# Performance work log

Measured on AMD Instinct MI355X. Metric: run time of the kernel, lower is better.

Reference implementation:

```python
import math
import jax, jax.numpy as jnp
import numpy as np

MAX_ATOMS_PER_BB = 8

def _sinusoidal_pe(d_model, max_len):
    # Faithful port of SinusoidalPositionalEmbedding buffer construction.
    position = jnp.arange(max_len, dtype=jnp.float32)[:, None]          # (L,1)
    div_term = jnp.exp(jnp.arange(0, d_model, 2, dtype=jnp.float32) * -(math.log(10000.0) / d_model))
    n_even = math.ceil(d_model / 2)
    n_odd = d_model - n_even
    pe = jnp.zeros((max_len, d_model), dtype=jnp.float32)
    pe = pe.at[:, 0::2].set(jnp.sin(position * div_term[:n_even]))
    pe = pe.at[:, 1::2].set(jnp.cos(position * div_term[:n_odd]))
    return pe

def setup_inputs() -> dict:
    key = jax.random.key(0)
    k1, k2, k3, k4 = jax.random.split(key, 4)
    bs, n, dy, dc = 8, 32, 64, 256
    E = jax.random.normal(k1, (bs, n, n, dy), dtype=jnp.float32)
    e_mask1 = (jax.random.uniform(k2, (bs, n, 1, 1)) > 0.2).astype(jnp.float32)
    e_mask2 = (jax.random.uniform(k3, (bs, 1, n, 1)) > 0.2).astype(jnp.float32)
    W = jax.random.normal(k4, (dc, dy), dtype=jnp.float32) * (1.0 / math.sqrt(dy))
    return {"E": E, "e_mask1": e_mask1, "e_mask2": e_mask2, "W": W}

def reference(E, e_mask1, e_mask2, W):
    M = MAX_ATOMS_PER_BB
    bs, n, _, dy = E.shape
    nm = n * M
    # Positional embedding table indexed by arange(M*M).reshape(M,M) -> (M,M,dy)
    pe = _sinusoidal_pe(dy, M * M).reshape(M, M, dy)
    # Masks: note original flattening orders (n,M) for mask1 but (M,n) for mask2.
    mask1 = jnp.broadcast_to(e_mask1, (bs, n, M, 1)).reshape(bs, nm, 1, 1)
    mask2 = jnp.broadcast_to(e_mask2, (bs, M, n, 1)).reshape(bs, 1, nm, 1)
    mask = mask1 * mask2                                             # (bs,nm,nm,1)
    # Broadcast E (bs,n,1,n,1,dy) + pe (1,1,M,1,M,dy) -> (bs,n,M,n,M,dy)
    Eb = E[:, :, None, :, None, :] + pe[None, None, :, None, :, :]
    E_masked = Eb.reshape(bs, nm, nm, dy) * mask
    out = jnp.einsum('bijd,cd->bijc', E_masked, W)                    # (bs,nm,nm,dc)
    return out
```

## Files before the change

### kernel.cpp

```cpp
#include <hip/hip_runtime.h>
#include <math.h>

typedef float f32x4 __attribute__((ext_vector_type(4)));


__global__ __launch_bounds__(256) void prep_kernel(const float* __restrict__ W,
                                                   float* __restrict__ Cpe,
                                                   float* __restrict__ Wt) {
    const int pos = blockIdx.x;
    const int t   = threadIdx.x;
    Wt[pos * 256 + t] = W[t * 64 + pos];
    __shared__ float peL[64];
    if (t < 64) {
        const float k2  = (float)(t & ~1);
        const float div = expf(-k2 * (logf(10000.0f) / 64.0f));
        const float arg = (float)pos * div;
        peL[t] = (t & 1) ? cosf(arg) : sinf(arg);
    }
    __syncthreads();
    const f32x4* W4 = (const f32x4*)W;
    float acc = 0.0f;
#pragma unroll
    for (int d4 = 0; d4 < 16; ++d4) {
        f32x4 w = W4[t * 16 + d4];
        acc += w.x * peL[4 * d4 + 0] + w.y * peL[4 * d4 + 1] +
               w.z * peL[4 * d4 + 2] + w.w * peL[4 * d4 + 3];
    }
    Cpe[pos * 256 + t] = acc;
}

__global__ __launch_bounds__(256) void etoc_stream(const float* __restrict__ E,
                                                   const float* __restrict__ m1p,
                                                   const float* __restrict__ m2p,
                                                   const float* __restrict__ Wt,
                                                   const float* __restrict__ Cpe,
                                                   float* __restrict__ out) {
    const int blk = blockIdx.x;
    const int h = blk & 1;
    const int i = (blk >> 1) & 31;
    const int b = blk >> 6;
    const int t = threadIdx.x;
    const int w = t >> 6;
    const int g = t & 63;
    const int j0 = h * 16 + w * 4;

    const f32x4* Wt4 = (const f32x4*)Wt;
    const f32x4* E4  = (const f32x4*)E;
    const int ebase = ((b * 32 + i) * 32 + j0) * 16;
    f32x4 acc0 = {0,0,0,0}, acc1 = {0,0,0,0}, acc2 = {0,0,0,0}, acc3 = {0,0,0,0};
#pragma unroll 4
    for (int d4 = 0; d4 < 16; ++d4) {
        const f32x4 e0 = E4[ebase + 0 * 16 + d4];
        const f32x4 e1 = E4[ebase + 1 * 16 + d4];
        const f32x4 e2 = E4[ebase + 2 * 16 + d4];
        const f32x4 e3 = E4[ebase + 3 * 16 + d4];
#pragma unroll
        for (int dd = 0; dd < 4; ++dd) {
            const f32x4 wv = Wt4[(d4 * 4 + dd) * 64 + g];
            acc0 += wv * e0[dd];
            acc1 += wv * e1[dd];
            acc2 += wv * e2[dd];
            acc3 += wv * e3[dd];
        }
    }

    const float m1v = m1p[b * 32 + i];
    f32x4 mm[8];
    const f32x4* m2v = (const f32x4*)(m2p + b * 32);
#pragma unroll
    for (int k = 0; k < 8; ++k) mm[k] = m2v[k] * m1v;

    const f32x4* Cpe4 = (const f32x4*)Cpe;
    f32x4* out4 = (f32x4*)out;
    const size_t rowb = ((size_t)(b * 256 + i * 8) * 256 + (size_t)j0 * 8);

#pragma unroll 1
    for (int a = 0; a < 8; ++a) {
        f32x4 q[8];
#pragma unroll
        for (int c = 0; c < 8; ++c) q[c] = Cpe4[(a * 8 + c) * 64 + g];
#pragma unroll
        for (int jl = 0; jl < 4; ++jl) {
            const f32x4 ce = (jl == 0) ? acc0 : (jl == 1) ? acc1 : (jl == 2) ? acc2 : acc3;
            const size_t base = (rowb + (size_t)a * 256 + (size_t)jl * 8) * 64 + (size_t)g;
#pragma unroll
            for (int c = 0; c < 8; ++c) {
                const float m = mm[2 * jl + (c >> 2)][c & 3];
                f32x4 r = (ce + q[c]) * m;
                out4[base + (size_t)c * 64] = r;
            }
        }
    }
}

extern "C" void kernel_launch(void* const* d_in, const int* in_sizes, int n_in,
                              void* d_out, int out_size, void* d_ws, size_t ws_size,
                              hipStream_t stream) {
    const float* E   = (const float*)d_in[0];
    const float* m1p = (const float*)d_in[1];
    const float* m2p = (const float*)d_in[2];
    const float* W   = (const float*)d_in[3];
    float* out = (float*)d_out;

    float* Cpe = (float*)d_ws;
    float* Wt  = (float*)((char*)d_ws + 65536);

    prep_kernel<<<64, 256, 0, stream>>>(W, Cpe, Wt);
    etoc_stream<<<512, 256, 0, stream>>>(E, m1p, m2p, Wt, Cpe, out);
}
```

Baseline: 110.3 us.

## Split output rows across blocks with per-block pe row and nontemporal stores

Each block now owns one (b, i, a) output row instead of a (b, i, half) slice that looped over all 8 a-values. Each wave handles 8 j columns, so the E×W projection is recomputed 8× more often across blocks. In exchange there are 4× more blocks, contiguous 64 KB row writes and one Cpe load per block. Block IDs are swizzled so that blocks with the same (b, i) are spread out. Output writes use nontemporal stores to avoid polluting the cache. The trade-off is more redundant FMA work and E reads against better parallelism and store streaming.

```diff
diff --git a/kernel.cpp b/kernel.cpp
--- a/kernel.cpp
+++ b/kernel.cpp
@@ -35,32 +35,31 @@
                                                    const float* __restrict__ Wt,
                                                    const float* __restrict__ Cpe,
                                                    float* __restrict__ out) {
-    const int blk = blockIdx.x;
-    const int h = blk & 1;
-    const int i = (blk >> 1) & 31;
-    const int b = blk >> 6;
+    const int bid = blockIdx.x;
+    const int blk = (bid & 7) * 256 + (bid >> 3);
+    const int ii = blk & 255;
+    const int b  = blk >> 8;
+    const int i = ii >> 3, a = ii & 7;
     const int t = threadIdx.x;
     const int w = t >> 6;
     const int g = t & 63;
-    const int j0 = h * 16 + w * 4;
 
     const f32x4* Wt4 = (const f32x4*)Wt;
     const f32x4* E4  = (const f32x4*)E;
-    const int ebase = ((b * 32 + i) * 32 + j0) * 16;
-    f32x4 acc0 = {0,0,0,0}, acc1 = {0,0,0,0}, acc2 = {0,0,0,0}, acc3 = {0,0,0,0};
+    const int ebase = ((b * 32 + i) * 32 + w * 8) * 16;
+    f32x4 acc[8];
+#pragma unroll
+    for (int jl = 0; jl < 8; ++jl) acc[jl] = (f32x4){0, 0, 0, 0};
 #pragma unroll 4
     for (int d4 = 0; d4 < 16; ++d4) {
-        const f32x4 e0 = E4[ebase + 0 * 16 + d4];
-        const f32x4 e1 = E4[ebase + 1 * 16 + d4];
-        const f32x4 e2 = E4[ebase + 2 * 16 + d4];
-        const f32x4 e3 = E4[ebase + 3 * 16 + d4];
+        f32x4 e[8];
+#pragma unroll
+        for (int jl = 0; jl < 8; ++jl) e[jl] = E4[ebase + jl * 16 + d4];
 #pragma unroll
         for (int dd = 0; dd < 4; ++dd) {
             const f32x4 wv = Wt4[(d4 * 4 + dd) * 64 + g];
-            acc0 += wv * e0[dd];
-            acc1 += wv * e1[dd];
-            acc2 += wv * e2[dd];
-            acc3 += wv * e3[dd];
+#pragma unroll
+            for (int jl = 0; jl < 8; ++jl) acc[jl] += wv * e[jl][dd];
         }
     }
 
@@ -71,25 +70,19 @@
     for (int k = 0; k < 8; ++k) mm[k] = m2v[k] * m1v;
 
     const f32x4* Cpe4 = (const f32x4*)Cpe;
+    f32x4 q[8];
+#pragma unroll
+    for (int c = 0; c < 8; ++c) q[c] = Cpe4[(a * 8 + c) * 64 + g];
+
     f32x4* out4 = (f32x4*)out;
-    const size_t rowb = ((size_t)(b * 256 + i * 8) * 256 + (size_t)j0 * 8);
-
-#pragma unroll 1
-    for (int a = 0; a < 8; ++a) {
-        f32x4 q[8];
+    const size_t base = ((size_t)blk * 256 + (size_t)w * 64) * 64 + (size_t)g;
 #pragma unroll
-        for (int c = 0; c < 8; ++c) q[c] = Cpe4[(a * 8 + c) * 64 + g];
-#pragma unroll
-        for (int jl = 0; jl < 4; ++jl) {
-            const f32x4 ce = (jl == 0) ? acc0 : (jl == 1) ? acc1 : (jl == 2) ? acc2 : acc3;
-            const size_t base = (rowb + (size_t)a * 256 + (size_t)jl * 8) * 64 + (size_t)g;
-#pragma unroll
-            for (int c = 0; c < 8; ++c) {
-                const float m = mm[2 * jl + (c >> 2)][c & 3];
-                f32x4 r = (ce + q[c]) * m;
-                out4[base + (size_t)c * 64] = r;
-            }
-        }
+    for (int r = 0; r < 64; ++r) {
+        const int jl = r >> 3;
+        const int c  = r & 7;
+        const int mr = r & 31;
+        const f32x4 v = (acc[jl] + q[c]) * mm[mr >> 2][mr & 3];
+        __builtin_nontemporal_store(v, &out4[base + (size_t)r * 64]);
     }
 }
 
@@ -106,5 +99,5 @@
     float* Wt  = (float*)((char*)d_ws + 65536);
 
     prep_kernel<<<64, 256, 0, stream>>>(W, Cpe, Wt);
-    etoc_stream<<<512, 256, 0, stream>>>(E, m1p, m2p, Wt, Cpe, out);
+    etoc_stream<<<2048, 256, 0, stream>>>(E, m1p, m2p, Wt, Cpe, out);
 }
```

New measurement: 121.6 us. 10.2% more time.
